# Kernel tuning notes

Hardware: AMD Instinct MI355X
Metric: run time of the kernel (lower is better)

Reference implementation:

```python
import jax, jax.numpy as jnp
import numpy as np

B, S, D, DS = 8, 2048, 1024, 64
TEMP = 1.0  # surprise_temp
IMP_TH, SUR_TH = 0.5, 0.7


def _l2norm(x):
    # F.normalize(dim=-1): x / max(||x||, 1e-12)
    return x / jnp.maximum(jnp.linalg.norm(x, axis=-1, keepdims=True), 1e-12)


def setup_inputs() -> dict:
    key = jax.random.key(0)
    ks = jax.random.split(key, 12)
    s = 0.02
    return {
        "x": jax.random.normal(ks[0], (B, S, D), jnp.float32),
        "Wk": jax.random.normal(ks[1], (DS, D), jnp.float32) * s,
        "Wv": jax.random.normal(ks[2], (DS, D), jnp.float32) * s,
        "Wq": jax.random.normal(ks[3], (DS, D), jnp.float32) * s,
        "fast_alpha": jnp.float32(0.8),
        "slow_alpha": jnp.float32(0.99),
        "nm_w1": jax.random.normal(ks[4], (2 * DS, DS), jnp.float32) * s,
        "nm_b1": jnp.zeros((2 * DS,), jnp.float32),
        "nm_w2": jax.random.normal(ks[5], (DS, 2 * DS), jnp.float32) * s,
        "nm_b2": jnp.zeros((DS,), jnp.float32),
        "ir_w1": jax.random.normal(ks[6], (DS, D), jnp.float32) * s,
        "ir_b1": jnp.zeros((DS,), jnp.float32),
        "ir_w2": jax.random.normal(ks[7], (1, DS), jnp.float32) * s,
        "ir_b2": jnp.zeros((1,), jnp.float32),
        "pw": jax.random.normal(ks[8], (3, D), jnp.float32) * s,
        "Wo": jax.random.normal(ks[9], (D, DS), jnp.float32) * s,
        "norm_w": jnp.ones((DS,), jnp.float32),
    }


def reference(x, Wk, Wv, Wq, fast_alpha, slow_alpha, nm_w1, nm_b1, nm_w2, nm_b2,
              ir_w1, ir_b1, ir_w2, ir_b2, pw, Wo, norm_w):
    Bb = x.shape[0]
    k = _l2norm(x @ Wk.T)                      # [B,S,DS]
    v = x @ Wv.T                               # [B,S,DS]
    q = _l2norm(x @ Wq.T)                      # [B,S,DS]
    # Stateless per-token quantities, precomputed outside the scan:
    imp = jax.nn.sigmoid(jax.nn.gelu(x @ ir_w1.T + ir_b1, approximate=False) @ ir_w2.T + ir_b2)  # [B,S,1]
    nu = jax.nn.gelu(v @ nm_w1.T + nm_b1, approximate=False) @ nm_w2.T + nm_b2                    # [B,S,DS]
    pwt = jax.nn.softmax(x @ pw.T, axis=-1)                                                       # [B,S,3]

    def step(carry, inp):
        fH, sH, ns = carry                     # [B,DS,DS],[B,DS,DS],[B,DS]
        k_t, v_t, q_t, i_t, nu_t, p_t = inp    # [B,DS],[B,DS],[B,DS],[B,1],[B,DS],[B,3]
        # surprise from prediction error against pre-update states
        pred = (jnp.einsum('bk,bkv->bv', q_t, fH) + jnp.einsum('bk,bkv->bv', q_t, sH)) * 0.5
        err = jnp.sum((v_t - pred) ** 2, axis=-1, keepdims=True)       # [B,1]
        surprise = jax.nn.sigmoid(err / (TEMP + 1e-6))
        kv = k_t[:, :, None] * v_t[:, None, :]                         # [B,DS,DS]
        # fast path: delta rule, always updated
        d_fast = kv - k_t[:, :, None] * jnp.einsum('bk,bkv->bv', k_t, fH)[:, None, :]
        fH = fast_alpha * fH + (1 - fast_alpha) * d_fast
        # slow path: gated by importance threshold
        u_slow = (i_t > IMP_TH).astype(x.dtype)                        # [B,1]
        d_slow = kv - k_t[:, :, None] * jnp.einsum('bk,bkv->bv', k_t, sH)[:, None, :]
        sH = slow_alpha * sH + (1 - slow_alpha) * u_slow[:, :, None] * d_slow
        # neural memory: gated by surprise threshold
        u_neu = (surprise > SUR_TH).astype(x.dtype)                    # [B,1]
        ns = ns + u_neu * (nu_t - ns) * 0.1
        o = (p_t[:, 0:1] * jnp.einsum('bk,bkv->bv', q_t, fH)
             + p_t[:, 1:2] * jnp.einsum('bk,bkv->bv', q_t, sH)
             + p_t[:, 2:3] * ns)
        return (fH, sH, ns), o

    ds = Wk.shape[0]
    init = (jnp.zeros((Bb, ds, ds), x.dtype),
            jnp.zeros((Bb, ds, ds), x.dtype),
            jnp.zeros((Bb, ds), x.dtype))
    xs = (k.transpose(1, 0, 2), v.transpose(1, 0, 2), q.transpose(1, 0, 2),
          imp.transpose(1, 0, 2), nu.transpose(1, 0, 2), pwt.transpose(1, 0, 2))
    _, out = jax.lax.scan(step, init, xs)      # [S,B,DS]
    out = out.transpose(1, 0, 2)               # [B,S,DS]
    # RMSNorm in fp32
    of = out.astype(jnp.float32)
    of = of * jax.lax.rsqrt(jnp.mean(of * of, axis=-1, keepdims=True) + 1e-6)
    out = (of * norm_w).astype(out.dtype)
    return out @ Wo.T                          # [B,S,D]
```

## Files before the change

kernel.cpp:

```cpp
#include <hip/hip_runtime.h>
#include <hip/hip_bf16.h>
#include <math.h>

#define BB 8
#define SS 2048
#define DD 1024
#define DS 64
#define MM (BB*SS)

typedef __attribute__((ext_vector_type(8))) short short8b;
typedef __attribute__((ext_vector_type(4))) float f32x4;


__device__ __forceinline__ float4 ld4(const float* p) { return *(const float4*)p; }

template<int CTRL>
__device__ __forceinline__ float dppadd(float x) {
  int v = __builtin_amdgcn_update_dpp(0, __float_as_int(x), CTRL, 0xf, 0xf, true);
  return x + __int_as_float(v);
}

__device__ __forceinline__ float xor16add(float x) {
#if defined(__has_builtin) && __has_builtin(__builtin_amdgcn_permlane16_swap)
  auto r = __builtin_amdgcn_permlane16_swap(__float_as_uint(x), __float_as_uint(x), false, false);
  return __uint_as_float(r[0]) + __uint_as_float(r[1]);
#else
  return x + __shfl_xor(x, 16, 64);
#endif
}
__device__ __forceinline__ float xor32add(float x) {
#if defined(__has_builtin) && __has_builtin(__builtin_amdgcn_permlane32_swap)
  auto r = __builtin_amdgcn_permlane32_swap(__float_as_uint(x), __float_as_uint(x), false, false);
  return __uint_as_float(r[0]) + __uint_as_float(r[1]);
#else
  return x + __shfl_xor(x, 32, 64);
#endif
}

__device__ __forceinline__ float wsum(float x) {
  x = dppadd<0xB1>(x);
  x = dppadd<0x4E>(x);
  x = dppadd<0x141>(x);
  x = dppadd<0x140>(x);
  x = xor16add(x);
  x = xor32add(x);
  return x;
}

__device__ __forceinline__ float gelu_exact(float x) {
  return 0.5f * x * (1.f + erff(x * 0.7071067811865476f));
}

__device__ __forceinline__ void cvt8(const float* f, uint* hi, uint* lo) {
  #pragma unroll
  for (int i = 0; i < 4; ++i) {
    uint u0 = __float_as_uint(f[2*i]);
    uint u1 = __float_as_uint(f[2*i+1]);
    uint h0 = u0 & 0xFFFF0000u, h1 = u1 & 0xFFFF0000u;
    float l0 = f[2*i]   - __uint_as_float(h0);
    float l1 = f[2*i+1] - __uint_as_float(h1);
    hi[i] = (h0 >> 16) | h1;
    lo[i] = (__float_as_uint(l0) >> 16) | (__float_as_uint(l1) & 0xFFFF0000u);
  }
}

__global__ __launch_bounds__(256) void pack_w(
    const float* __restrict__ Wk, const float* __restrict__ Wv,
    const float* __restrict__ Wq, const float* __restrict__ ir_w1,
    const float* __restrict__ pw, float* __restrict__ Wcat) {
  int idx = blockIdx.x * 256 + threadIdx.x;
  int r = idx >> 10, c = idx & 1023;
  float val = 0.f;
  if (r < 64)       val = Wk[r*1024 + c];
  else if (r < 128) val = Wv[(r-64)*1024 + c];
  else if (r < 192) val = Wq[(r-128)*1024 + c];
  else if (r < 256) val = ir_w1[(r-192)*1024 + c];
  else if (r < 259) val = pw[(r-256)*1024 + c];
  Wcat[idx] = val;
}

__global__ __launch_bounds__(256) void gemm1(
    const float* __restrict__ X, const float* __restrict__ Wcat,
    float* __restrict__ Y) {
  __shared__ unsigned short Ah[128*64], Al[128*64];
  __shared__ unsigned short Bh[64*64],  Bl[64*64];
  const int t  = threadIdx.x;
  const int m0 = blockIdx.x * 128;
  const int n0 = blockIdx.y * 64;
  const int l  = t & 63, w = t >> 6;
  const int wm = (w >> 1) * 64, wn = (w & 1) * 32;
  const int fr = l & 15;
  const int fkb = (l >> 4) * 16;
  const int mA = t >> 1, khA = (t & 1) * 32;
  const int nB = t >> 2, kqB = (t & 3) * 16;
  f32x4 acc[4][2];
  #pragma unroll
  for (int i = 0; i < 4; ++i)
    #pragma unroll
    for (int j = 0; j < 2; ++j) acc[i][j] = (f32x4){0.f,0.f,0.f,0.f};

  for (int k0 = 0; k0 < 1024; k0 += 64) {
    __syncthreads();
    {
      const float* src = X + (size_t)(m0 + mA)*1024 + k0 + khA;
      float f[32];
      #pragma unroll
      for (int j = 0; j < 8; ++j) *(float4*)&f[j*4] = ld4(src + j*4);
      #pragma unroll
      for (int g = 0; g < 4; ++g) {
        uint hi[4], lo[4];
        cvt8(&f[g*8], hi, lo);
        int off = mA*128 + ((khA*2 + g*16) ^ ((mA & 7) << 4));
        *(uint4*)((char*)Ah + off) = make_uint4(hi[0],hi[1],hi[2],hi[3]);
        *(uint4*)((char*)Al + off) = make_uint4(lo[0],lo[1],lo[2],lo[3]);
      }
    }
    {
      const float* src = Wcat + (size_t)(n0 + nB)*1024 + k0 + kqB;
      float f[16];
      #pragma unroll
      for (int j = 0; j < 4; ++j) *(float4*)&f[j*4] = ld4(src + j*4);
      #pragma unroll
      for (int g = 0; g < 2; ++g) {
        uint hi[4], lo[4];
        cvt8(&f[g*8], hi, lo);
        int off = nB*128 + ((kqB*2 + g*16) ^ ((nB & 7) << 4));
        *(uint4*)((char*)Bh + off) = make_uint4(hi[0],hi[1],hi[2],hi[3]);
        *(uint4*)((char*)Bl + off) = make_uint4(lo[0],lo[1],lo[2],lo[3]);
      }
    }
    __syncthreads();
    #pragma unroll
    for (int h = 0; h < 2; ++h) {
      const int kb = h*64 + fkb;
      short8b ah[4], al[4], bh[2], bl[2];
      #pragma unroll
      for (int i = 0; i < 4; ++i) {
        int row = wm + i*16 + fr;
        int off = row*128 + (kb ^ ((row & 7) << 4));
        ah[i] = *(const short8b*)((const char*)Ah + off);
        al[i] = *(const short8b*)((const char*)Al + off);
      }
      #pragma unroll
      for (int j = 0; j < 2; ++j) {
        int row = wn + j*16 + fr;
        int off = row*128 + (kb ^ ((row & 7) << 4));
        bh[j] = *(const short8b*)((const char*)Bh + off);
        bl[j] = *(const short8b*)((const char*)Bl + off);
      }
      #pragma unroll
      for (int i = 0; i < 4; ++i)
        #pragma unroll
        for (int j = 0; j < 2; ++j) {
          acc[i][j] = __builtin_amdgcn_mfma_f32_16x16x32_bf16(ah[i], bh[j], acc[i][j], 0, 0, 0);
          acc[i][j] = __builtin_amdgcn_mfma_f32_16x16x32_bf16(ah[i], bl[j], acc[i][j], 0, 0, 0);
          acc[i][j] = __builtin_amdgcn_mfma_f32_16x16x32_bf16(al[i], bh[j], acc[i][j], 0, 0, 0);
        }
    }
  }
  #pragma unroll
  for (int i = 0; i < 4; ++i)
    #pragma unroll
    for (int j = 0; j < 2; ++j)
      #pragma unroll
      for (int r = 0; r < 4; ++r) {
        int row = m0 + wm + i*16 + (l >> 4)*4 + r;
        int col = n0 + wn + j*16 + (l & 15);
        Y[(size_t)row*320 + col] = acc[i][j][r];
      }
}

__global__ __launch_bounds__(256) void post_kernel(
    const float* __restrict__ Y,
    const float* __restrict__ nm_w1, const float* __restrict__ nm_b1,
    const float* __restrict__ nm_w2, const float* __restrict__ nm_b2,
    const float* __restrict__ ir_b1, const float* __restrict__ ir_w2,
    const float* __restrict__ ir_b2, const float* __restrict__ sap,
    float* __restrict__ K, float* __restrict__ V, float* __restrict__ Q,
    float* __restrict__ NU, float* __restrict__ PW,
    float* __restrict__ SCL8) {
  __shared__ float w1s[128*65];
  __shared__ float w2s[64*129];
  __shared__ float vbuf[4][64];
  __shared__ float h1buf[4][128];
  const int tid = threadIdx.x, wid = tid >> 6, l = tid & 63;
  for (int i = tid; i < 128*64; i += 256) w1s[(i>>6)*65 + (i&63)]  = nm_w1[i];
  for (int i = tid; i < 64*128; i += 256) w2s[(i>>7)*129 + (i&127)] = nm_w2[i];
  __syncthreads();
  const float sa   = *sap;
  const float b1a  = nm_b1[l], b1b = nm_b1[64+l], b2l = nm_b2[l];
  const float irb1 = ir_b1[l], irw2 = ir_w2[l],  irb2 = ir_b2[0];
  for (int r = 0; r < 4; ++r) {
    const int tok = blockIdx.x*16 + r*4 + wid;
    const float* yr = Y + (size_t)tok*320;
    float kr = yr[l], vr = yr[64+l], qr = yr[128+l], hr = yr[192+l];
    float rk = 1.f / fmaxf(sqrtf(wsum(kr*kr)), 1e-12f);
    float rq = 1.f / fmaxf(sqrtf(wsum(qr*qr)), 1e-12f);
    float kn = kr*rk, qn = qr*rq;
    float qk = wsum(kn*qn);
    float g  = gelu_exact(hr + irb1);
    float logit = wsum(g*irw2) + irb2;
    float imp = 1.f/(1.f+expf(-logit));
    float bs  = (imp > 0.5f) ? (1.f - sa) : 0.f;
    K[(size_t)tok*64+l] = kn; V[(size_t)tok*64+l] = vr; Q[(size_t)tok*64+l] = qn;
    vbuf[wid][l] = vr;
    __syncthreads();
    float h1a = b1a, h1b = b1b;
    #pragma unroll 8
    for (int c = 0; c < 64; ++c) {
      float vv = vbuf[wid][c];
      h1a = fmaf(w1s[l*65 + c], vv, h1a);
      h1b = fmaf(w1s[(64+l)*65 + c], vv, h1b);
    }
    h1buf[wid][l]    = gelu_exact(h1a);
    h1buf[wid][64+l] = gelu_exact(h1b);
    __syncthreads();
    float nu = b2l;
    #pragma unroll 8
    for (int j = 0; j < 128; ++j) nu = fmaf(w2s[l*129 + j], h1buf[wid][j], nu);
    NU[(size_t)tok*64+l] = nu;
    float p0 = yr[256], p1 = yr[257], p2 = yr[258];
    float mx = fmaxf(p0, fmaxf(p1, p2));
    float e0 = expf(p0-mx), e1 = expf(p1-mx), e2 = expf(p2-mx);
    float inv = 1.f/(e0+e1+e2);
    if (l == 0) {
      PW[(size_t)tok*3]   = e0*inv;
      float4 s; s.x = qk; s.y = bs; s.z = e0*inv; s.w = e1*inv;
      *(float4*)&SCL8[(size_t)tok*8] = s;
    }
    else if (l == 1)   PW[(size_t)tok*3+1] = e1*inv;
    else if (l == 2)   PW[(size_t)tok*3+2] = e2*inv;
    __syncthreads();
  }
}

#define STAGE68(dst, srcp) { _Pragma("unroll")                        \
    for (int it_ = 0; it_ < 4; ++it_) {                               \
      int idx4 = (threadIdx.x + it_*256)*4;                           \
      int r_ = idx4 >> 6; int d_ = idx4 & 63;                         \
      *(float4*)&dst[r_*68+d_] = ld4(&(srcp)[r_*64 + d_]); } }

__global__ __launch_bounds__(256) void chunkdots(
    const float* __restrict__ K, const float* __restrict__ Q,
    float* __restrict__ AKK, float* __restrict__ AQK) {
  __shared__ float Kl[64*68], Ql[64*68];
  const int tid = threadIdx.x;
  const size_t base = (size_t)blockIdx.x * 4096;
  STAGE68(Kl, K + base)
  STAGE68(Ql, Q + base)
  __syncthreads();
  const int t0 = (tid >> 4) * 4, j0 = (tid & 15) * 4;
  float akk[4][4], aqk[4][4];
  #pragma unroll
  for (int i = 0; i < 4; ++i)
    #pragma unroll
    for (int j = 0; j < 4; ++j) { akk[i][j] = 0.f; aqk[i][j] = 0.f; }
  for (int d = 0; d < 64; ++d) {
    float kt[4], qt[4], kj[4];
    #pragma unroll
    for (int i = 0; i < 4; ++i) {
      kt[i] = Kl[(t0+i)*68 + d];
      qt[i] = Ql[(t0+i)*68 + d];
      kj[i] = Kl[(j0+i)*68 + d];
    }
    #pragma unroll
    for (int i = 0; i < 4; ++i)
      #pragma unroll
      for (int j = 0; j < 4; ++j) {
        akk[i][j] = fmaf(kt[i], kj[j], akk[i][j]);
        aqk[i][j] = fmaf(qt[i], kj[j], aqk[i][j]);
      }
  }
  #pragma unroll
  for (int i = 0; i < 4; ++i) {
    float4 a; a.x=akk[i][0]; a.y=akk[i][1]; a.z=akk[i][2]; a.w=akk[i][3];
    float4 b; b.x=aqk[i][0]; b.y=aqk[i][1]; b.z=aqk[i][2]; b.w=aqk[i][3];
    *(float4*)&AKK[base + (t0+i)*64 + j0] = a;
    *(float4*)&AQK[base + (t0+i)*64 + j0] = b;
  }
}

__global__ __launch_bounds__(256) void pass1_solve(
    const float* __restrict__ K, const float* __restrict__ V,
    const float* __restrict__ SCL8, const float* __restrict__ AKK,
    const float* __restrict__ fap, const float* __restrict__ sap,
    float* __restrict__ Pf, float* __restrict__ Rf,
    float* __restrict__ Ps, float* __restrict__ Rs) {
  __shared__ float Mf[64*68], Ms[64*68];
  __shared__ float Xpf[64*68], Xrf[64*68], Xps[64*68], Xrs[64*68];
  __shared__ float bsv[64];
  __shared__ float fpw[65], spw[65];
  const int tid = threadIdx.x;
  const size_t chunk = blockIdx.x;
  const size_t tok0 = chunk * 64;
  const float fa = *fap, sa = *sap, omfa = 1.f - fa;
  if (tid == 0) {
    float f = 1.f, s = 1.f;
    for (int n = 0; n <= 64; ++n) { fpw[n] = f; spw[n] = s; f *= fa; s *= sa; }
  }
  STAGE68(Xpf, K + tok0*64)
  STAGE68(Xrf, V + tok0*64)
  STAGE68(Mf, AKK + chunk*4096)
  if (tid < 64) bsv[tid] = SCL8[(tok0 + tid)*8 + 1];
  __syncthreads();
  {
    const int t = tid >> 2, j0 = (tid & 3) * 16;
    const float bst = bsv[t];
    const float cpf = omfa*fpw[t], cps = bst*spw[t];
    #pragma unroll
    for (int i = 0; i < 16; ++i) {
      int j = j0 + i;
      float a    = Mf [t*68 + j];
      float kraw = Xpf[t*68 + j];
      float vraw = Xrf[t*68 + j];
      bool lt = (j < t);
      int p = lt ? (t-1-j) : 0;
      Ms [t*68 + j] = lt ? bst*spw[p]*a  : 0.f;
      Mf [t*68 + j] = lt ? omfa*fpw[p]*a : 0.f;
      Xps[t*68 + j] = cps * kraw;
      Xpf[t*68 + j] = cpf * kraw;
      Xrs[t*68 + j] = bst * vraw;
      Xrf[t*68 + j] = omfa * vraw;
    }
  }
  __syncthreads();

  const int g  = tid >> 6;
  const int cc = tid & 63;
  const float* M = (g < 2) ? Mf : Ms;
  float* X = (g == 0) ? Xpf : (g == 1) ? Xrf : (g == 2) ? Xps : Xrs;
  for (int t = 1; t < 64; ++t) {
    float a0 = 0.f, a1 = 0.f, a2 = 0.f, a3 = 0.f;
    int j = 0;
    for (; j + 4 <= t; j += 4) {
      float4 m = *(const float4*)&M[t*68 + j];
      a0 = fmaf(m.x, X[(j+0)*68 + cc], a0);
      a1 = fmaf(m.y, X[(j+1)*68 + cc], a1);
      a2 = fmaf(m.z, X[(j+2)*68 + cc], a2);
      a3 = fmaf(m.w, X[(j+3)*68 + cc], a3);
    }
    for (; j < t; ++j) a0 = fmaf(M[t*68 + j], X[j*68 + cc], a0);
    X[t*68 + cc] -= ((a0 + a1) + (a2 + a3));
  }
  float* dst = (g == 0) ? Pf : (g == 1) ? Rf : (g == 2) ? Ps : Rs;
  const size_t base = chunk*4096 + cc;
  for (int t = 0; t < 64; ++t) dst[base + t*64] = X[t*68 + cc];
}

__global__ __launch_bounds__(256) void pass1b_gh(
    const float* __restrict__ K,
    const float* __restrict__ Pf, const float* __restrict__ Rf,
    const float* __restrict__ Ps, const float* __restrict__ Rs,
    const float* __restrict__ fap, const float* __restrict__ sap,
    float* __restrict__ Gf, float* __restrict__ Hf,
    float* __restrict__ Gs, float* __restrict__ Hs) {
  __shared__ float Kc[64*68], Pl[64*68], Rl[64*68];
  __shared__ float dpw[65];
  const int tid = threadIdx.x;
  const size_t chunk = blockIdx.x >> 1;
  const int path = blockIdx.x & 1;
  const float d = path ? (*sap) : (*fap);
  if (tid == 0) {
    float p = 1.f;
    for (int n = 0; n <= 64; ++n) { dpw[n] = p; p *= d; }
  }
  const float* Pg = path ? Ps : Pf;
  const float* Rg = path ? Rs : Rf;
  float* Gg = path ? Gs : Gf;
  float* Hg = path ? Hs : Hf;
  STAGE68(Kc, K + chunk*4096)
  STAGE68(Pl, Pg + chunk*4096)
  STAGE68(Rl, Rg + chunk*4096)
  __syncthreads();
  const int kd = tid >> 2, c0 = (tid & 3) * 16;
  float accG[16], accH[16];
  #pragma unroll
  for (int i = 0; i < 16; ++i) { accG[i] = 0.f; accH[i] = 0.f; }
  #pragma unroll 8
  for (int j = 0; j < 64; ++j) {
    const float w = Kc[j*68 + kd] * dpw[63 - j];
    #pragma unroll
    for (int i4 = 0; i4 < 4; ++i4) {
      float4 p = *(const float4*)&Pl[j*68 + c0 + i4*4];
      float4 r = *(const float4*)&Rl[j*68 + c0 + i4*4];
      accG[i4*4+0] = fmaf(w, p.x, accG[i4*4+0]);
      accG[i4*4+1] = fmaf(w, p.y, accG[i4*4+1]);
      accG[i4*4+2] = fmaf(w, p.z, accG[i4*4+2]);
      accG[i4*4+3] = fmaf(w, p.w, accG[i4*4+3]);
      accH[i4*4+0] = fmaf(w, r.x, accH[i4*4+0]);
      accH[i4*4+1] = fmaf(w, r.y, accH[i4*4+1]);
      accH[i4*4+2] = fmaf(w, r.z, accH[i4*4+2]);
      accH[i4*4+3] = fmaf(w, r.w, accH[i4*4+3]);
    }
  }
  const float d64 = dpw[64];
  #pragma unroll
  for (int i4 = 0; i4 < 4; ++i4) {
    float4 go, ho;
    float* gp = (float*)&go; float* hp = (float*)&ho;
    #pragma unroll
    for (int i = 0; i < 4; ++i) {
      int col = c0 + i4*4 + i;
      gp[i] = ((col == kd) ? d64 : 0.f) - accG[i4*4+i];
      hp[i] = accH[i4*4+i];
    }
    *(float4*)&Gg[chunk*4096 + (size_t)kd*64 + c0 + i4*4] = go;
    *(float4*)&Hg[chunk*4096 + (size_t)kd*64 + c0 + i4*4] = ho;
  }
}

__global__ __launch_bounds__(256) void pass2_rec(
    const float* __restrict__ Gf, const float* __restrict__ Hf,
    const float* __restrict__ Gs, const float* __restrict__ Hs,
    float* __restrict__ Fstf, float* __restrict__ Fsts) {
  __shared__ float Fl[64*36], Gl[64*68], Hl[64*36];
  const int tid = threadIdx.x;
  const int b = blockIdx.x >> 2;
  const int path = (blockIdx.x >> 1) & 1;
  const int vh = blockIdx.x & 1;
  const float* Gg = path ? Gs : Gf;
  const float* Hg = path ? Hs : Hf;
  float* Fstg = path ? Fsts : Fstf;
  const int kd = tid >> 2, vq = tid & 3;
  #pragma unroll
  for (int i = 0; i < 8; ++i) Fl[kd*36 + vq*8 + i] = 0.f;
  __syncthreads();
  for (int c = 0; c < 32; ++c) {
    const size_t chunk = (size_t)b*32 + c;
    STAGE68(Gl, Gg + chunk*4096)
    *(float4*)&Hl[kd*36 + vq*8]     = ld4(&Hg[chunk*4096 + kd*64 + vh*32 + vq*8]);
    *(float4*)&Hl[kd*36 + vq*8 + 4] = ld4(&Hg[chunk*4096 + kd*64 + vh*32 + vq*8 + 4]);
    *(float4*)&Fstg[chunk*4096 + (size_t)kd*64 + vh*32 + vq*8]     = *(float4*)&Fl[kd*36 + vq*8];
    *(float4*)&Fstg[chunk*4096 + (size_t)kd*64 + vh*32 + vq*8 + 4] = *(float4*)&Fl[kd*36 + vq*8 + 4];
    __syncthreads();
    float acc[8];
    #pragma unroll
    for (int i = 0; i < 8; ++i) acc[i] = Hl[kd*36 + vq*8 + i];
    #pragma unroll 8
    for (int j = 0; j < 64; ++j) {
      const float g = Gl[kd*68 + j];
      float4 f0 = *(const float4*)&Fl[j*36 + vq*8];
      float4 f1 = *(const float4*)&Fl[j*36 + vq*8 + 4];
      acc[0]=fmaf(g,f0.x,acc[0]); acc[1]=fmaf(g,f0.y,acc[1]);
      acc[2]=fmaf(g,f0.z,acc[2]); acc[3]=fmaf(g,f0.w,acc[3]);
      acc[4]=fmaf(g,f1.x,acc[4]); acc[5]=fmaf(g,f1.y,acc[5]);
      acc[6]=fmaf(g,f1.z,acc[6]); acc[7]=fmaf(g,f1.w,acc[7]);
    }
    __syncthreads();
    #pragma unroll
    for (int i = 0; i < 8; ++i) Fl[kd*36 + vq*8 + i] = acc[i];
    __syncthreads();
  }
}

__global__ __launch_bounds__(256) void pass3_out(
    const float* __restrict__ Q, const float* __restrict__ V,
    const float* __restrict__ SCL8, const float* __restrict__ AQK,
    const float* __restrict__ Pf, const float* __restrict__ Rf,
    const float* __restrict__ Ps, const float* __restrict__ Rs,
    const float* __restrict__ Fstf, const float* __restrict__ Fsts,
    const float* __restrict__ fap, const float* __restrict__ sap,
    float* __restrict__ OBASE, float* __restrict__ E2) {
  __shared__ float Qcl[64*68], AQKl[64*68], Pfl[64*68], Psl[64*68];
  __shared__ float Vl[64*36], Rfl[64*36], Rsl[64*36];
  __shared__ float F0l[64*36], S0l[64*36], Ufl[64*36], Usl[64*36];
  __shared__ float scal[256];
  __shared__ float fpw[65], spw[65];
  const int tid = threadIdx.x;
  const size_t chunk = blockIdx.x >> 1;
  const int vh = blockIdx.x & 1;
  const size_t tok0 = chunk * 64;
  const float fa = *fap, sa = *sap;
  if (tid == 0) {
    float f = 1.f, s = 1.f;
    for (int n = 0; n <= 64; ++n) { fpw[n] = f; spw[n] = s; f *= fa; s *= sa; }
  }
  STAGE68(Qcl,  Q   + tok0*64)
  STAGE68(AQKl, AQK + chunk*4096)
  STAGE68(Pfl,  Pf  + chunk*4096)
  STAGE68(Psl,  Ps  + chunk*4096)
  {
    const int r = tid >> 2, vq = tid & 3;
    const size_t off = chunk*4096 + (size_t)r*64 + vh*32 + vq*8;
    *(float4*)&Vl [r*36 + vq*8]     = ld4(&V   [tok0*64 + (size_t)r*64 + vh*32 + vq*8]);
    *(float4*)&Vl [r*36 + vq*8 + 4] = ld4(&V   [tok0*64 + (size_t)r*64 + vh*32 + vq*8 + 4]);
    *(float4*)&Rfl[r*36 + vq*8]     = ld4(&Rf  [off]);
    *(float4*)&Rfl[r*36 + vq*8 + 4] = ld4(&Rf  [off + 4]);
    *(float4*)&Rsl[r*36 + vq*8]     = ld4(&Rs  [off]);
    *(float4*)&Rsl[r*36 + vq*8 + 4] = ld4(&Rs  [off + 4]);
    *(float4*)&F0l[r*36 + vq*8]     = ld4(&Fstf[off]);
    *(float4*)&F0l[r*36 + vq*8 + 4] = ld4(&Fstf[off + 4]);
    *(float4*)&S0l[r*36 + vq*8]     = ld4(&Fsts[off]);
    *(float4*)&S0l[r*36 + vq*8 + 4] = ld4(&Fsts[off + 4]);
    scal[tid] = SCL8[(tok0 + r)*8 + vq];
  }
  __syncthreads();
  {
    const int j = tid >> 2, vq = tid & 3;
    float uf[8], us[8];
    #pragma unroll
    for (int i = 0; i < 8; ++i) { uf[i] = 0.f; us[i] = 0.f; }
    #pragma unroll 8
    for (int kd = 0; kd < 64; ++kd) {
      const float pfv = Pfl[j*68 + kd];
      const float psv = Psl[j*68 + kd];
      float4 f0 = *(const float4*)&F0l[kd*36 + vq*8];
      float4 f1 = *(const float4*)&F0l[kd*36 + vq*8 + 4];
      float4 s0 = *(const float4*)&S0l[kd*36 + vq*8];
      float4 s1 = *(const float4*)&S0l[kd*36 + vq*8 + 4];
      uf[0]=fmaf(pfv,f0.x,uf[0]); uf[1]=fmaf(pfv,f0.y,uf[1]);
      uf[2]=fmaf(pfv,f0.z,uf[2]); uf[3]=fmaf(pfv,f0.w,uf[3]);
      uf[4]=fmaf(pfv,f1.x,uf[4]); uf[5]=fmaf(pfv,f1.y,uf[5]);
      uf[6]=fmaf(pfv,f1.z,uf[6]); uf[7]=fmaf(pfv,f1.w,uf[7]);
      us[0]=fmaf(psv,s0.x,us[0]); us[1]=fmaf(psv,s0.y,us[1]);
      us[2]=fmaf(psv,s0.z,us[2]); us[3]=fmaf(psv,s0.w,us[3]);
      us[4]=fmaf(psv,s1.x,us[4]); us[5]=fmaf(psv,s1.y,us[5]);
      us[6]=fmaf(psv,s1.z,us[6]); us[7]=fmaf(psv,s1.w,us[7]);
    }
    #pragma unroll
    for (int i = 0; i < 8; ++i) {
      Ufl[j*36 + vq*8 + i] = Rfl[j*36 + vq*8 + i] - uf[i];
      Usl[j*36 + vq*8 + i] = Rsl[j*36 + vq*8 + i] - us[i];
    }
  }
  __syncthreads();
  {
    const int t = tid >> 2, vq = tid & 3;
    float af[8], as_[8];
    #pragma unroll
    for (int i = 0; i < 8; ++i) { af[i] = 0.f; as_[i] = 0.f; }
    #pragma unroll 8
    for (int kd = 0; kd < 64; ++kd) {
      const float q = Qcl[t*68 + kd];
      float4 f0 = *(const float4*)&F0l[kd*36 + vq*8];
      float4 f1 = *(const float4*)&F0l[kd*36 + vq*8 + 4];
      float4 s0 = *(const float4*)&S0l[kd*36 + vq*8];
      float4 s1 = *(const float4*)&S0l[kd*36 + vq*8 + 4];
      af[0]=fmaf(q,f0.x,af[0]); af[1]=fmaf(q,f0.y,af[1]);
      af[2]=fmaf(q,f0.z,af[2]); af[3]=fmaf(q,f0.w,af[3]);
      af[4]=fmaf(q,f1.x,af[4]); af[5]=fmaf(q,f1.y,af[5]);
      af[6]=fmaf(q,f1.z,af[6]); af[7]=fmaf(q,f1.w,af[7]);
      as_[0]=fmaf(q,s0.x,as_[0]); as_[1]=fmaf(q,s0.y,as_[1]);
      as_[2]=fmaf(q,s0.z,as_[2]); as_[3]=fmaf(q,s0.w,as_[3]);
      as_[4]=fmaf(q,s1.x,as_[4]); as_[5]=fmaf(q,s1.y,as_[5]);
      as_[6]=fmaf(q,s1.z,as_[6]); as_[7]=fmaf(q,s1.w,as_[7]);
    }
    float pq[8], pqs[8];
    #pragma unroll
    for (int i = 0; i < 8; ++i) { pq[i] = fpw[t]*af[i]; pqs[i] = spw[t]*as_[i]; }
    for (int j = 0; j < 64; ++j) {
      const float aq = AQKl[t*68 + j];
      const bool lt = (j < t);
      const int p = lt ? (t-1-j) : 0;
      const float wf = lt ? fpw[p]*aq : 0.f;
      const float ws = lt ? spw[p]*aq : 0.f;
      float4 u0 = *(const float4*)&Ufl[j*36 + vq*8];
      float4 u1 = *(const float4*)&Ufl[j*36 + vq*8 + 4];
      float4 w0 = *(const float4*)&Usl[j*36 + vq*8];
      float4 w1 = *(const float4*)&Usl[j*36 + vq*8 + 4];
      pq[0]=fmaf(wf,u0.x,pq[0]); pq[1]=fmaf(wf,u0.y,pq[1]);
      pq[2]=fmaf(wf,u0.z,pq[2]); pq[3]=fmaf(wf,u0.w,pq[3]);
      pq[4]=fmaf(wf,u1.x,pq[4]); pq[5]=fmaf(wf,u1.y,pq[5]);
      pq[6]=fmaf(wf,u1.z,pq[6]); pq[7]=fmaf(wf,u1.w,pq[7]);
      pqs[0]=fmaf(ws,w0.x,pqs[0]); pqs[1]=fmaf(ws,w0.y,pqs[1]);
      pqs[2]=fmaf(ws,w0.z,pqs[2]); pqs[3]=fmaf(ws,w0.w,pqs[3]);
      pqs[4]=fmaf(ws,w1.x,pqs[4]); pqs[5]=fmaf(ws,w1.y,pqs[5]);
      pqs[6]=fmaf(ws,w1.z,pqs[6]); pqs[7]=fmaf(ws,w1.w,pqs[7]);
    }
    const float qk = scal[t*4+0], p0 = scal[t*4+2], p1 = scal[t*4+3];
    float ob[8], ee[8];
    #pragma unroll
    for (int i = 0; i < 8; ++i) {
      const float uft = Ufl[t*36 + vq*8 + i];
      const float ust = Usl[t*36 + vq*8 + i];
      const float qfn = fmaf(fa, pq[i],  qk*uft);
      const float qsn = fmaf(sa, pqs[i], qk*ust);
      ob[i] = fmaf(p0, qfn, p1*qsn);
      const float pd = Vl[t*36 + vq*8 + i] - 0.5f*(pq[i] + pqs[i]);
      ee[i] = pd*pd;
    }
    const size_t o = (tok0 + t)*64 + vh*32 + vq*8;
    *(float4*)&OBASE[o]     = *(float4*)&ob[0];
    *(float4*)&OBASE[o + 4] = *(float4*)&ob[4];
    *(float4*)&E2[o]        = *(float4*)&ee[0];
    *(float4*)&E2[o + 4]    = *(float4*)&ee[4];
  }
}

__global__ __launch_bounds__(256) void err_kernel(
    const float* __restrict__ E, float* __restrict__ CNS) {
  int row = blockIdx.x*4 + (threadIdx.x >> 6);
  int l = threadIdx.x & 63;
  float s = wsum(E[(size_t)row*64 + l]);
  if (l == 0) {
    float z = s / (1.0f + 1e-6f);
    float sg = 1.f/(1.f+expf(-z));
    CNS[row] = (sg > 0.7f) ? 0.1f : 0.f;
  }
}

__global__ __launch_bounds__(64) void nsseg(
    const float* __restrict__ CNS, const float* __restrict__ NU,
    float* __restrict__ ASEG, float* __restrict__ BSEG) {
  const int bseg = blockIdx.x;
  const int v = threadIdx.x;
  const size_t t0 = (size_t)(bseg) * 64;
  float a = 1.f, bv = 0.f;
  for (int i = 0; i < 64; ++i) {
    float c  = CNS[t0 + i];
    float nu = NU[(t0 + i)*64 + v];
    bv = fmaf(1.f - c, bv, c*nu);
    a *= (1.f - c);
  }
  BSEG[(size_t)bseg*64 + v] = bv;
  if (v == 0) ASEG[bseg] = a;
}

__global__ __launch_bounds__(64) void nspre(
    const float* __restrict__ ASEG, const float* __restrict__ BSEG,
    float* __restrict__ NSST) {
  const int b = blockIdx.x, v = threadIdx.x;
  float ns = 0.f;
  for (int s = 0; s < 32; ++s) {
    const int bs = b*32 + s;
    NSST[(size_t)bs*64 + v] = ns;
    ns = fmaf(ASEG[bs], ns, BSEG[(size_t)bs*64 + v]);
  }
}

__global__ __launch_bounds__(64) void nsout2(
    const float* __restrict__ CNS, const float* __restrict__ NU,
    const float* __restrict__ OBASE, const float* __restrict__ PW,
    const float* __restrict__ NSST, float* __restrict__ OB) {
  const int bseg = blockIdx.x;
  const int v = threadIdx.x;
  const size_t t0 = (size_t)bseg * 64;
  float ns = NSST[(size_t)bseg*64 + v];
  for (int i = 0; i < 64; ++i) {
    float c  = CNS[t0 + i];
    float nu = NU[(t0 + i)*64 + v];
    ns = fmaf(1.f - c, ns, c*nu);
    OB[(t0 + i)*64 + v] = fmaf(PW[(t0 + i)*3 + 2], ns, OBASE[(t0 + i)*64 + v]);
  }
}

__global__ __launch_bounds__(256) void out_gemm(
    const float* __restrict__ OB, const float* __restrict__ Wo,
    const float* __restrict__ normw, float* __restrict__ out) {
  __shared__ float As[64*64];
  __shared__ float Bs[64*128];
  const int t  = threadIdx.x;
  const int m0 = blockIdx.y * 64;
  const int n0 = blockIdx.x * 128;
  {
    int r = t >> 2, q4 = t & 3;
    const float* src = OB + (size_t)(m0 + r)*64 + q4*16;
    float4 x0 = ld4(src), x1 = ld4(src+4), x2 = ld4(src+8), x3 = ld4(src+12);
    float ss = x0.x*x0.x+x0.y*x0.y+x0.z*x0.z+x0.w*x0.w
             + x1.x*x1.x+x1.y*x1.y+x1.z*x1.z+x1.w*x1.w
             + x2.x*x2.x+x2.y*x2.y+x2.z*x2.z+x2.w*x2.w
             + x3.x*x3.x+x3.y*x3.y+x3.z*x3.z+x3.w*x3.w;
    ss += __shfl_xor(ss, 1, 64);
    ss += __shfl_xor(ss, 2, 64);
    float rms = rsqrtf(ss * (1.f/64.f) + 1e-6f);
    const float* nw = normw + q4*16;
    float4 w0 = ld4(nw), w1 = ld4(nw+4), w2 = ld4(nw+8), w3 = ld4(nw+12);
    int kbase = q4*16;
    As[(kbase+ 0)*64+r]=x0.x*rms*w0.x; As[(kbase+ 1)*64+r]=x0.y*rms*w0.y;
    As[(kbase+ 2)*64+r]=x0.z*rms*w0.z; As[(kbase+ 3)*64+r]=x0.w*rms*w0.w;
    As[(kbase+ 4)*64+r]=x1.x*rms*w1.x; As[(kbase+ 5)*64+r]=x1.y*rms*w1.y;
    As[(kbase+ 6)*64+r]=x1.z*rms*w1.z; As[(kbase+ 7)*64+r]=x1.w*rms*w1.w;
    As[(kbase+ 8)*64+r]=x2.x*rms*w2.x; As[(kbase+ 9)*64+r]=x2.y*rms*w2.y;
    As[(kbase+10)*64+r]=x2.z*rms*w2.z; As[(kbase+11)*64+r]=x2.w*rms*w2.w;
    As[(kbase+12)*64+r]=x3.x*rms*w3.x; As[(kbase+13)*64+r]=x3.y*rms*w3.y;
    As[(kbase+14)*64+r]=x3.z*rms*w3.z; As[(kbase+15)*64+r]=x3.w*rms*w3.w;
  }
  {
    int rw = t >> 1, half = t & 1;
    const float* src = Wo + (size_t)(n0 + rw)*64 + half*32;
    #pragma unroll
    for (int j = 0; j < 8; ++j) {
      float4 w = ld4(src + j*4);
      int k = half*32 + j*4;
      Bs[(k+0)*128+rw] = w.x; Bs[(k+1)*128+rw] = w.y;
      Bs[(k+2)*128+rw] = w.z; Bs[(k+3)*128+rw] = w.w;
    }
  }
  __syncthreads();
  const int mi = t >> 5, ni = t & 31;
  float acc[8][4];
  #pragma unroll
  for (int i = 0; i < 8; ++i)
    #pragma unroll
    for (int j = 0; j < 4; ++j) acc[i][j] = 0.f;
  #pragma unroll 8
  for (int k = 0; k < 64; ++k) {
    float a[8], bv[4];
    float4 a0 = *(const float4*)&As[k*64 + mi*8];
    float4 a1 = *(const float4*)&As[k*64 + mi*8 + 4];
    float4 b0 = *(const float4*)&Bs[k*128 + ni*4];
    a[0]=a0.x; a[1]=a0.y; a[2]=a0.z; a[3]=a0.w;
    a[4]=a1.x; a[5]=a1.y; a[6]=a1.z; a[7]=a1.w;
    bv[0]=b0.x; bv[1]=b0.y; bv[2]=b0.z; bv[3]=b0.w;
    #pragma unroll
    for (int im = 0; im < 8; ++im)
      #pragma unroll
      for (int in = 0; in < 4; ++in)
        acc[im][in] = fmaf(a[im], bv[in], acc[im][in]);
  }
  #pragma unroll
  for (int im = 0; im < 8; ++im) {
    float4 o; o.x=acc[im][0]; o.y=acc[im][1]; o.z=acc[im][2]; o.w=acc[im][3];
    *(float4*)&out[(size_t)(m0 + mi*8 + im)*1024 + n0 + ni*4] = o;
  }
}

extern "C" void kernel_launch(void* const* d_in, const int* in_sizes, int n_in,
                              void* d_out, int out_size, void* d_ws, size_t ws_size,
                              hipStream_t stream) {
  const float* x     = (const float*)d_in[0];
  const float* Wk    = (const float*)d_in[1];
  const float* Wv    = (const float*)d_in[2];
  const float* Wq    = (const float*)d_in[3];
  const float* fap   = (const float*)d_in[4];
  const float* sap   = (const float*)d_in[5];
  const float* nm_w1 = (const float*)d_in[6];
  const float* nm_b1 = (const float*)d_in[7];
  const float* nm_w2 = (const float*)d_in[8];
  const float* nm_b2 = (const float*)d_in[9];
  const float* ir_w1 = (const float*)d_in[10];
  const float* ir_b1 = (const float*)d_in[11];
  const float* ir_w2 = (const float*)d_in[12];
  const float* ir_b2 = (const float*)d_in[13];
  const float* pw    = (const float*)d_in[14];
  const float* Wo    = (const float*)d_in[15];
  const float* normw = (const float*)d_in[16];
  float* out = (float*)d_out;
  float* ws  = (float*)d_ws;

  const size_t oW    = 0;
  const size_t oY    = oW + (size_t)320*1024;
  const size_t oOBASE = oY;
  const size_t oE     = oY + (size_t)1*MM*64;
  const size_t oPfA   = oY + (size_t)2*MM*64;
  const size_t oAQK   = oY + (size_t)3*MM*64;
  const size_t oPs    = oY + (size_t)4*MM*64;
  const size_t oK    = oY + (size_t)MM*320;
  const size_t oV    = oK + (size_t)MM*64;
  const size_t oQ    = oV + (size_t)MM*64;
  const size_t oNU   = oQ + (size_t)MM*64;
  const size_t oPW   = oNU + (size_t)MM*64;
  const size_t oSCL  = oPW + (size_t)MM*3;
  const size_t oCNS  = oSCL + (size_t)MM*8;
  const size_t oOB   = oCNS + MM;
  const size_t oRf   = oOB  + (size_t)MM*64;
  const size_t oRs   = oRf  + (size_t)MM*64;
  const size_t oGf   = oRs  + (size_t)MM*64;
  const size_t oGs   = oGf  + (size_t)MM*64;
  const size_t oHf   = oGs  + (size_t)MM*64;
  const size_t oHs   = oHf  + (size_t)MM*64;
  const size_t oFstf = oHs  + (size_t)MM*64;
  const size_t oFsts = oFstf + (size_t)MM*64;
  const size_t oASEG = oFsts + (size_t)MM*64;
  const size_t oBSEG = oASEG + 256;
  const size_t oNSST = oBSEG + 16384;

  pack_w<<<1280, 256, 0, stream>>>(Wk, Wv, Wq, ir_w1, pw, ws + oW);
  gemm1<<<dim3(128, 5), 256, 0, stream>>>(x, ws + oW, ws + oY);
  post_kernel<<<1024, 256, 0, stream>>>(ws + oY,
                                        nm_w1, nm_b1, nm_w2, nm_b2,
                                        ir_b1, ir_w2, ir_b2, sap,
                                        ws + oK, ws + oV, ws + oQ, ws + oNU,
                                        ws + oPW, ws + oSCL);
  chunkdots<<<256, 256, 0, stream>>>(ws + oK, ws + oQ, ws + oPfA, ws + oAQK);
  pass1_solve<<<256, 256, 0, stream>>>(ws + oK, ws + oV, ws + oSCL, ws + oPfA,
                                       fap, sap,
                                       ws + oPfA, ws + oRf, ws + oPs, ws + oRs);
  pass1b_gh<<<512, 256, 0, stream>>>(ws + oK,
                                     ws + oPfA, ws + oRf, ws + oPs, ws + oRs,
                                     fap, sap,
                                     ws + oGf, ws + oHf, ws + oGs, ws + oHs);
  pass2_rec<<<32, 256, 0, stream>>>(ws + oGf, ws + oHf, ws + oGs, ws + oHs,
                                    ws + oFstf, ws + oFsts);
  pass3_out<<<512, 256, 0, stream>>>(ws + oQ, ws + oV, ws + oSCL, ws + oAQK,
                                     ws + oPfA, ws + oRf, ws + oPs, ws + oRs,
                                     ws + oFstf, ws + oFsts, fap, sap,
                                     ws + oOBASE, ws + oE);
  err_kernel<<<4096, 256, 0, stream>>>(ws + oE, ws + oCNS);
  nsseg<<<256, 64, 0, stream>>>(ws + oCNS, ws + oNU, ws + oASEG, ws + oBSEG);
  nspre<<<8, 64, 0, stream>>>(ws + oASEG, ws + oBSEG, ws + oNSST);
  nsout2<<<256, 64, 0, stream>>>(ws + oCNS, ws + oNU, ws + oOBASE, ws + oPW,
                                 ws + oNSST, ws + oOB);
  out_gemm<<<dim3(8, 256), 256, 0, stream>>>(ws + oOB, Wo, normw, out);
}
```

Measured before the change: 366.8 us.

## Split gemm1 over K halves and widen pass2 recurrence over value columns

gemm1 now launches with a z-dimension of two, so each block reduces half of the K range and writes partial results to two buffers (the second reuses the Rf workspace region). post_kernel sums the two partials when it loads them. Separately, pass2_rec splits the value dimension into four 16-column slices instead of two 32-column halves, doubling its grid from 32 to 64 blocks. Both changes are meant to fill more of the GPU's compute units during launches that were too small to occupy it. The cost is extra partial-sum traffic in gemm1/post_kernel and more redundant G staging per block in pass2_rec.

```diff
diff --git a/kernel.cpp b/kernel.cpp
--- a/kernel.cpp
+++ b/kernel.cpp
@@ -81,12 +81,13 @@
 
 __global__ __launch_bounds__(256) void gemm1(
     const float* __restrict__ X, const float* __restrict__ Wcat,
-    float* __restrict__ Y) {
+    float* __restrict__ YP0, float* __restrict__ YP1) {
   __shared__ unsigned short Ah[128*64], Al[128*64];
   __shared__ unsigned short Bh[64*64],  Bl[64*64];
   const int t  = threadIdx.x;
   const int m0 = blockIdx.x * 128;
   const int n0 = blockIdx.y * 64;
+  const int kh0 = blockIdx.z * 512;
   const int l  = t & 63, w = t >> 6;
   const int wm = (w >> 1) * 64, wn = (w & 1) * 32;
   const int fr = l & 15;
@@ -99,7 +100,7 @@
     #pragma unroll
     for (int j = 0; j < 2; ++j) acc[i][j] = (f32x4){0.f,0.f,0.f,0.f};
 
-  for (int k0 = 0; k0 < 1024; k0 += 64) {
+  for (int k0 = kh0; k0 < kh0 + 512; k0 += 64) {
     __syncthreads();
     {
       const float* src = X + (size_t)(m0 + mA)*1024 + k0 + khA;
@@ -158,6 +159,7 @@
         }
     }
   }
+  float* Y = blockIdx.z ? YP1 : YP0;
   #pragma unroll
   for (int i = 0; i < 4; ++i)
     #pragma unroll
@@ -171,7 +173,7 @@
 }
 
 __global__ __launch_bounds__(256) void post_kernel(
-    const float* __restrict__ Y,
+    const float* __restrict__ YP0, const float* __restrict__ YP1,
     const float* __restrict__ nm_w1, const float* __restrict__ nm_b1,
     const float* __restrict__ nm_w2, const float* __restrict__ nm_b2,
     const float* __restrict__ ir_b1, const float* __restrict__ ir_w2,
@@ -192,8 +194,12 @@
   const float irb1 = ir_b1[l], irw2 = ir_w2[l],  irb2 = ir_b2[0];
   for (int r = 0; r < 4; ++r) {
     const int tok = blockIdx.x*16 + r*4 + wid;
-    const float* yr = Y + (size_t)tok*320;
-    float kr = yr[l], vr = yr[64+l], qr = yr[128+l], hr = yr[192+l];
+    const float* yr0 = YP0 + (size_t)tok*320;
+    const float* yr1 = YP1 + (size_t)tok*320;
+    float kr = yr0[l]     + yr1[l];
+    float vr = yr0[64+l]  + yr1[64+l];
+    float qr = yr0[128+l] + yr1[128+l];
+    float hr = yr0[192+l] + yr1[192+l];
     float rk = 1.f / fmaxf(sqrtf(wsum(kr*kr)), 1e-12f);
     float rq = 1.f / fmaxf(sqrtf(wsum(qr*qr)), 1e-12f);
     float kn = kr*rk, qn = qr*rq;
@@ -219,7 +225,9 @@
     #pragma unroll 8
     for (int j = 0; j < 128; ++j) nu = fmaf(w2s[l*129 + j], h1buf[wid][j], nu);
     NU[(size_t)tok*64+l] = nu;
-    float p0 = yr[256], p1 = yr[257], p2 = yr[258];
+    float p0 = yr0[256] + yr1[256];
+    float p1 = yr0[257] + yr1[257];
+    float p2 = yr0[258] + yr1[258];
     float mx = fmaxf(p0, fmaxf(p1, p2));
     float e0 = expf(p0-mx), e1 = expf(p1-mx), e2 = expf(p2-mx);
     float inv = 1.f/(e0+e1+e2);
@@ -413,42 +421,37 @@
     const float* __restrict__ Gf, const float* __restrict__ Hf,
     const float* __restrict__ Gs, const float* __restrict__ Hs,
     float* __restrict__ Fstf, float* __restrict__ Fsts) {
-  __shared__ float Fl[64*36], Gl[64*68], Hl[64*36];
+  __shared__ float Fl[64*20], Gl[64*68], Hl[64*20];
   const int tid = threadIdx.x;
-  const int b = blockIdx.x >> 2;
-  const int path = (blockIdx.x >> 1) & 1;
-  const int vh = blockIdx.x & 1;
+  const int b = blockIdx.x >> 3;
+  const int path = (blockIdx.x >> 2) & 1;
+  const int vq4 = blockIdx.x & 3;
   const float* Gg = path ? Gs : Gf;
   const float* Hg = path ? Hs : Hf;
   float* Fstg = path ? Fsts : Fstf;
-  const int kd = tid >> 2, vq = tid & 3;
-  #pragma unroll
-  for (int i = 0; i < 8; ++i) Fl[kd*36 + vq*8 + i] = 0.f;
+  const int kd = tid >> 2, vi = tid & 3;
+  #pragma unroll
+  for (int i = 0; i < 4; ++i) Fl[kd*20 + vi*4 + i] = 0.f;
   __syncthreads();
   for (int c = 0; c < 32; ++c) {
     const size_t chunk = (size_t)b*32 + c;
     STAGE68(Gl, Gg + chunk*4096)
-    *(float4*)&Hl[kd*36 + vq*8]     = ld4(&Hg[chunk*4096 + kd*64 + vh*32 + vq*8]);
-    *(float4*)&Hl[kd*36 + vq*8 + 4] = ld4(&Hg[chunk*4096 + kd*64 + vh*32 + vq*8 + 4]);
-    *(float4*)&Fstg[chunk*4096 + (size_t)kd*64 + vh*32 + vq*8]     = *(float4*)&Fl[kd*36 + vq*8];
-    *(float4*)&Fstg[chunk*4096 + (size_t)kd*64 + vh*32 + vq*8 + 4] = *(float4*)&Fl[kd*36 + vq*8 + 4];
+    *(float4*)&Hl[kd*20 + vi*4] = ld4(&Hg[chunk*4096 + kd*64 + vq4*16 + vi*4]);
+    *(float4*)&Fstg[chunk*4096 + (size_t)kd*64 + vq4*16 + vi*4] = *(float4*)&Fl[kd*20 + vi*4];
     __syncthreads();
-    float acc[8];
-    #pragma unroll
-    for (int i = 0; i < 8; ++i) acc[i] = Hl[kd*36 + vq*8 + i];
+    float acc[4];
+    #pragma unroll
+    for (int i = 0; i < 4; ++i) acc[i] = Hl[kd*20 + vi*4 + i];
     #pragma unroll 8
     for (int j = 0; j < 64; ++j) {
       const float g = Gl[kd*68 + j];
-      float4 f0 = *(const float4*)&Fl[j*36 + vq*8];
-      float4 f1 = *(const float4*)&Fl[j*36 + vq*8 + 4];
+      float4 f0 = *(const float4*)&Fl[j*20 + vi*4];
       acc[0]=fmaf(g,f0.x,acc[0]); acc[1]=fmaf(g,f0.y,acc[1]);
       acc[2]=fmaf(g,f0.z,acc[2]); acc[3]=fmaf(g,f0.w,acc[3]);
-      acc[4]=fmaf(g,f1.x,acc[4]); acc[5]=fmaf(g,f1.y,acc[5]);
-      acc[6]=fmaf(g,f1.z,acc[6]); acc[7]=fmaf(g,f1.w,acc[7]);
     }
     __syncthreads();
     #pragma unroll
-    for (int i = 0; i < 8; ++i) Fl[kd*36 + vq*8 + i] = acc[i];
+    for (int i = 0; i < 4; ++i) Fl[kd*20 + vi*4 + i] = acc[i];
     __syncthreads();
   }
 }
@@ -764,10 +767,11 @@
   const size_t oASEG = oFsts + (size_t)MM*64;
   const size_t oBSEG = oASEG + 256;
   const size_t oNSST = oBSEG + 16384;
+  const size_t oYP1 = oRf;
 
   pack_w<<<1280, 256, 0, stream>>>(Wk, Wv, Wq, ir_w1, pw, ws + oW);
-  gemm1<<<dim3(128, 5), 256, 0, stream>>>(x, ws + oW, ws + oY);
-  post_kernel<<<1024, 256, 0, stream>>>(ws + oY,
+  gemm1<<<dim3(128, 5, 2), 256, 0, stream>>>(x, ws + oW, ws + oY, ws + oYP1);
+  post_kernel<<<1024, 256, 0, stream>>>(ws + oY, ws + oYP1,
                                         nm_w1, nm_b1, nm_w2, nm_b2,
                                         ir_b1, ir_w2, ir_b2, sap,
                                         ws + oK, ws + oV, ws + oQ, ws + oNU,
@@ -780,7 +784,7 @@
                                      ws + oPfA, ws + oRf, ws + oPs, ws + oRs,
                                      fap, sap,
                                      ws + oGf, ws + oHf, ws + oGs, ws + oHs);
-  pass2_rec<<<32, 256, 0, stream>>>(ws + oGf, ws + oHf, ws + oGs, ws + oHs,
+  pass2_rec<<<64, 256, 0, stream>>>(ws + oGf, ws + oHf, ws + oGs, ws + oHs,
                                     ws + oFstf, ws + oFsts);
   pass3_out<<<512, 256, 0, stream>>>(ws + oQ, ws + oV, ws + oSCL, ws + oAQK,
                                      ws + oPfA, ws + oRf, ws + oPs, ws + oRs,
```

After: 341.8 us. 6.8% less time.
